# Performance work log

Hardware: AMD Instinct MI355X
Metric: run time of the kernel (lower is better)

The kernel has to match this reference:

```python
import jax, jax.numpy as jnp
import numpy as np

B, D, N = 4, 96, 512
ATTN = 256
OUT = 1


def setup_inputs() -> dict:
    key = jax.random.key(0)
    ks = jax.random.split(key, 4)
    x = jax.random.normal(ks[0], (B, D, N), dtype=jnp.float32)
    Wg1 = jax.random.normal(ks[1], (ATTN, D), dtype=jnp.float32) / np.sqrt(D)
    Wg2 = jax.random.normal(ks[2], (ATTN, D), dtype=jnp.float32) / np.sqrt(D)
    bg = jnp.zeros((ATTN,), dtype=jnp.float32)
    Wa_w = jax.random.normal(ks[3], (OUT, ATTN), dtype=jnp.float32) / np.sqrt(ATTN)
    Wa_b = jnp.zeros((OUT,), dtype=jnp.float32)
    ba = jnp.zeros((OUT,), dtype=jnp.float32)
    return {"x": x, "Wg1": Wg1, "Wg2": Wg2, "bg": bg, "Wa_w": Wa_w, "Wa_b": Wa_b, "ba": ba}


def reference(x, Wg1, Wg2, bg, Wa_w, Wa_b, ba):
    # x: (B, D, N) -> transpose to (B, N, D)
    xt = jnp.swapaxes(x, 1, 2)
    g1 = jnp.einsum("bnd,ad->bna", xt, Wg1)  # (B, N, ATTN)
    g2 = jnp.einsum("bnd,ad->bna", xt, Wg2)  # (B, N, ATTN)
    # pairwise additive scores: (B, N, N, ATTN)
    gnn = jnp.tanh(g1[:, :, None, :] + g2[:, None, :, :] + bg)
    # project to scalar per pair, add both biases (Wa bias and ba), sigmoid
    att = jax.nn.sigmoid(jnp.einsum("bnma,oa->bnmo", gnn, Wa_w) + Wa_b + ba)
    att = att.squeeze(-1)  # (B, N, N)
    return jnp.matmul(att, xt)  # (B, N, D)
```

## Files before the change

### kernel.cpp

```cpp
#include <hip/hip_runtime.h>
#include <math.h>

#define NB 4
#define ND 96
#define NN 512
#define NA 256

static constexpr float C_TANH = 2.8853900817779268f;
static constexpr float LOG2E  = 1.4426950408889634f;

__device__ __forceinline__ float fexp2(float x) {
#if __has_builtin(__builtin_amdgcn_exp2f)
  return __builtin_amdgcn_exp2f(x);
#else
  return exp2f(x);
#endif
}
__device__ __forceinline__ float frcp(float x) {
#if __has_builtin(__builtin_amdgcn_rcpf)
  return __builtin_amdgcn_rcpf(x);
#else
  return 1.0f / x;
#endif
}

__global__ __launch_bounds__(256) void k_prep(const float* __restrict__ Wg1,
                                              const float* __restrict__ Wg2,
                                              const float* __restrict__ Wa_w,
                                              const float* __restrict__ Wa_b,
                                              const float* __restrict__ ba,
                                              float* __restrict__ W1t,
                                              float* __restrict__ W2t,
                                              float* __restrict__ S0) {
  if (blockIdx.x == 192) {
    __shared__ float red[256];
    int t = threadIdx.x;
    red[t] = Wa_w[t];
    __syncthreads();
    for (int s = 128; s > 0; s >>= 1) {
      if (t < s) red[t] += red[t + s];
      __syncthreads();
    }
    if (t == 0) S0[0] = red[0] + Wa_b[0] + ba[0];
    return;
  }
  int idx = blockIdx.x * 256 + threadIdx.x;
  int mat = idx / (ND * NA);
  int rem = idx - mat * (ND * NA);
  int d = rem >> 8;
  int a = rem & 255;
  (mat ? W2t : W1t)[d * NA + a] = (mat ? Wg2 : Wg1)[a * ND + d];
}

__global__ __launch_bounds__(256, 2) void k_proj(const float* __restrict__ x,
                                                 const float* __restrict__ W1t,
                                                 const float* __restrict__ W2t,
                                                 const float* __restrict__ bg,
                                                 float* __restrict__ G1,
                                                 float* __restrict__ G2c,
                                                 float* __restrict__ xt) {
  __shared__ float4 xsh[ND];
  const int tid = threadIdx.x;
  const int b = blockIdx.x >> 7;
  const int n0 = (blockIdx.x & 127) * 4;

  for (int idx = tid; idx < ND * 4; idx += 256) {
    int d = idx >> 2, j = idx & 3;
    float v = x[(size_t)(b * ND + d) * NN + n0 + j];
    ((float*)&xsh[d])[j] = v;
    xt[(size_t)(b * NN + n0 + j) * ND + d] = v;
  }
  __syncthreads();

  const int a = tid;
  const float bgv = bg[a];
  float acc1[4], acc2[4];
#pragma unroll
  for (int j = 0; j < 4; ++j) { acc1[j] = bgv; acc2[j] = 0.f; }

  for (int d4 = 0; d4 < ND / 4; ++d4) {
    float w1[4], w2[4];
#pragma unroll
    for (int dd = 0; dd < 4; ++dd) {
      w1[dd] = W1t[(d4 * 4 + dd) * NA + a];
      w2[dd] = W2t[(d4 * 4 + dd) * NA + a];
    }
#pragma unroll
    for (int dd = 0; dd < 4; ++dd) {
      float4 xq = xsh[d4 * 4 + dd];
      float xv[4] = {xq.x, xq.y, xq.z, xq.w};
#pragma unroll
      for (int j = 0; j < 4; ++j) {
        acc1[j] = fmaf(w1[dd], xv[j], acc1[j]);
        acc2[j] = fmaf(w2[dd], xv[j], acc2[j]);
      }
    }
  }
  const int c = a >> 5, al = a & 31;
#pragma unroll
  for (int j = 0; j < 4; ++j) {
    G1[(size_t)(b * NN + n0 + j) * NA + a] = C_TANH * acc1[j];
    G2c[((size_t)(b * 8 + c) * NN + n0 + j) * 32 + al] = C_TANH * acc2[j];
  }
}

__global__ __launch_bounds__(256, 4) void k_main(const float* __restrict__ G1,
                                                 const float* __restrict__ G2c,
                                                 const float* __restrict__ xt,
                                                 const float* __restrict__ Wa_w,
                                                 const float* __restrict__ S0p,
                                                 float* __restrict__ out) {
  __shared__ float4 g2sh[256 * 8];
  __shared__ float attsh[4][NN];
  const int tid = threadIdx.x;
  const int b = blockIdx.x >> 7;
  const int n0 = (blockIdx.x & 127) << 2;
  const float S0 = S0p[0];
  const float4* __restrict__ W4 = (const float4*)Wa_w;
  const float* __restrict__ g1r0 = G1 + (size_t)(b * NN + n0) * NA;

  for (int p = 0; p < 2; ++p) {
    float acc[4] = {0.f, 0.f, 0.f, 0.f};
    for (int c = 0; c < 8; ++c) {
      const float4* __restrict__ src =
          (const float4*)(G2c + ((size_t)(b * 8 + c) * NN + p * 256) * 32);
      __syncthreads();
#pragma unroll
      for (int k = 0; k < 8; ++k) {
        int f = k * 256 + tid;
        int r = f >> 3, q = f & 7;
        g2sh[r * 8 + (q ^ (r & 7))] = src[f];
      }
      __syncthreads();
#pragma unroll
      for (int k4 = 0; k4 < 8; ++k4) {
        float4 v = g2sh[tid * 8 + (k4 ^ (tid & 7))];
        float g2v[4] = {v.x, v.y, v.z, v.w};
        float4 wq = W4[c * 8 + k4];
        float wv[4] = {wq.x, wq.y, wq.z, wq.w};
#pragma unroll
        for (int nl = 0; nl < 4; ++nl) {
          float4 g = *(const float4*)(g1r0 + nl * NA + c * 32 + k4 * 4);
          float g1v[4] = {g.x, g.y, g.z, g.w};
#pragma unroll
          for (int j = 0; j < 4; ++j) {
            float e = fexp2(g1v[j] + g2v[j]);
            acc[nl] = fmaf(wv[j], frcp(1.f + e), acc[nl]);
          }
        }
      }
    }
#pragma unroll
    for (int nl = 0; nl < 4; ++nl) {
      float z = S0 - 2.f * acc[nl];
      attsh[nl][p * 256 + tid] = frcp(1.f + fexp2(-LOG2E * z));
    }
  }
  __syncthreads();

  const int w = tid >> 6;
  const int l = tid & 63;
  const float* __restrict__ xb = xt + (size_t)b * NN * ND;
  const float* __restrict__ arow = attsh[w];
  float o0 = 0.f, o1 = 0.f;
  for (int m = 0; m < NN; ++m) {
    float av = arow[m];
    const float* xr = xb + m * ND;
    o0 = fmaf(av, xr[l], o0);
    o1 = fmaf(av, xr[64 + (l & 31)], o1);
  }
  float* orow = out + (size_t)(b * NN + n0 + w) * ND;
  orow[l] = o0;
  if (l < 32) orow[64 + l] = o1;
}

extern "C" void kernel_launch(void* const* d_in, const int* in_sizes, int n_in,
                              void* d_out, int out_size, void* d_ws, size_t ws_size,
                              hipStream_t stream) {
  const float* x    = (const float*)d_in[0];
  const float* Wg1  = (const float*)d_in[1];
  const float* Wg2  = (const float*)d_in[2];
  const float* bg   = (const float*)d_in[3];
  const float* Wa_w = (const float*)d_in[4];
  const float* Wa_b = (const float*)d_in[5];
  const float* ba   = (const float*)d_in[6];
  float* out = (float*)d_out;

  float* ws  = (float*)d_ws;
  float* G1  = ws;
  float* G2c = ws + 524288;
  float* xtw = ws + 1048576;
  float* W1t = ws + 1245184;
  float* W2t = ws + 1269760;
  float* S0  = ws + 1294336;

  hipLaunchKernelGGL(k_prep, dim3(193), dim3(256), 0, stream,
                     Wg1, Wg2, Wa_w, Wa_b, ba, W1t, W2t, S0);
  hipLaunchKernelGGL(k_proj, dim3(512), dim3(256), 0, stream,
                     x, W1t, W2t, bg, G1, G2c, xtw);
  hipLaunchKernelGGL(k_main, dim3(512), dim3(256), 0, stream,
                     G1, G2c, xtw, Wa_w, S0, out);
}
```

Measured before the change: 169.8 us.

## Split main kernel across m-quarters and attention halves with atomic output reduction

The weight-transpose prep kernel is removed. The projection kernel now reads Wg1/Wg2 rows directly as float4, and the Wa_w sum is computed inside the main kernel. The main kernel grid grows to four times as many blocks: each block handles a quarter of the m range, and its two thread halves each cover half of the attention dimension, reading G2 rows straight from global memory with no LDS staging. The two halves are combined through shared memory, and the partial att·x products are summed with atomicAdd into an output that is zeroed by a memset. This raises parallelism and occupancy, at the cost of extra atomics, a memset, and redundant per-thread weight sums.

```diff
diff --git a/kernel.cpp b/kernel.cpp
--- a/kernel.cpp
+++ b/kernel.cpp
@@ -24,40 +24,12 @@
 #endif
 }
 
-__global__ __launch_bounds__(256) void k_prep(const float* __restrict__ Wg1,
-                                              const float* __restrict__ Wg2,
-                                              const float* __restrict__ Wa_w,
-                                              const float* __restrict__ Wa_b,
-                                              const float* __restrict__ ba,
-                                              float* __restrict__ W1t,
-                                              float* __restrict__ W2t,
-                                              float* __restrict__ S0) {
-  if (blockIdx.x == 192) {
-    __shared__ float red[256];
-    int t = threadIdx.x;
-    red[t] = Wa_w[t];
-    __syncthreads();
-    for (int s = 128; s > 0; s >>= 1) {
-      if (t < s) red[t] += red[t + s];
-      __syncthreads();
-    }
-    if (t == 0) S0[0] = red[0] + Wa_b[0] + ba[0];
-    return;
-  }
-  int idx = blockIdx.x * 256 + threadIdx.x;
-  int mat = idx / (ND * NA);
-  int rem = idx - mat * (ND * NA);
-  int d = rem >> 8;
-  int a = rem & 255;
-  (mat ? W2t : W1t)[d * NA + a] = (mat ? Wg2 : Wg1)[a * ND + d];
-}
-
-__global__ __launch_bounds__(256, 2) void k_proj(const float* __restrict__ x,
-                                                 const float* __restrict__ W1t,
-                                                 const float* __restrict__ W2t,
+__global__ __launch_bounds__(256, 4) void k_proj(const float* __restrict__ x,
+                                                 const float* __restrict__ Wg1,
+                                                 const float* __restrict__ Wg2,
                                                  const float* __restrict__ bg,
                                                  float* __restrict__ G1,
-                                                 float* __restrict__ G2c,
+                                                 float* __restrict__ G2,
                                                  float* __restrict__ xt) {
   __shared__ float4 xsh[ND];
   const int tid = threadIdx.x;
@@ -66,81 +38,91 @@
 
   for (int idx = tid; idx < ND * 4; idx += 256) {
     int d = idx >> 2, j = idx & 3;
-    float v = x[(size_t)(b * ND + d) * NN + n0 + j];
-    ((float*)&xsh[d])[j] = v;
-    xt[(size_t)(b * NN + n0 + j) * ND + d] = v;
-  }
-  __syncthreads();
+    ((float*)&xsh[d])[j] = x[(size_t)(b * ND + d) * NN + n0 + j];
+  }
+  __syncthreads();
+  if (tid < ND) {
+    float4 v = xsh[tid];
+    xt[(size_t)(b * NN + n0 + 0) * ND + tid] = v.x;
+    xt[(size_t)(b * NN + n0 + 1) * ND + tid] = v.y;
+    xt[(size_t)(b * NN + n0 + 2) * ND + tid] = v.z;
+    xt[(size_t)(b * NN + n0 + 3) * ND + tid] = v.w;
+  }
 
   const int a = tid;
   const float bgv = bg[a];
-  float acc1[4], acc2[4];
-#pragma unroll
-  for (int j = 0; j < 4; ++j) { acc1[j] = bgv; acc2[j] = 0.f; }
-
+  float acc1[4] = {bgv, bgv, bgv, bgv};
+  float acc2[4] = {0.f, 0.f, 0.f, 0.f};
+  const float4* __restrict__ w1p = (const float4*)(Wg1 + (size_t)a * ND);
+  const float4* __restrict__ w2p = (const float4*)(Wg2 + (size_t)a * ND);
+
+#pragma unroll 4
   for (int d4 = 0; d4 < ND / 4; ++d4) {
-    float w1[4], w2[4];
-#pragma unroll
-    for (int dd = 0; dd < 4; ++dd) {
-      w1[dd] = W1t[(d4 * 4 + dd) * NA + a];
-      w2[dd] = W2t[(d4 * 4 + dd) * NA + a];
-    }
+    float4 w1 = w1p[d4], w2 = w2p[d4];
+    float w1c[4] = {w1.x, w1.y, w1.z, w1.w};
+    float w2c[4] = {w2.x, w2.y, w2.z, w2.w};
 #pragma unroll
     for (int dd = 0; dd < 4; ++dd) {
       float4 xq = xsh[d4 * 4 + dd];
       float xv[4] = {xq.x, xq.y, xq.z, xq.w};
 #pragma unroll
       for (int j = 0; j < 4; ++j) {
-        acc1[j] = fmaf(w1[dd], xv[j], acc1[j]);
-        acc2[j] = fmaf(w2[dd], xv[j], acc2[j]);
+        acc1[j] = fmaf(w1c[dd], xv[j], acc1[j]);
+        acc2[j] = fmaf(w2c[dd], xv[j], acc2[j]);
       }
     }
   }
-  const int c = a >> 5, al = a & 31;
 #pragma unroll
   for (int j = 0; j < 4; ++j) {
     G1[(size_t)(b * NN + n0 + j) * NA + a] = C_TANH * acc1[j];
-    G2c[((size_t)(b * 8 + c) * NN + n0 + j) * 32 + al] = C_TANH * acc2[j];
-  }
-}
-
-__global__ __launch_bounds__(256, 4) void k_main(const float* __restrict__ G1,
-                                                 const float* __restrict__ G2c,
+    G2[(size_t)(b * NN + n0 + j) * NA + a] = C_TANH * acc2[j];
+  }
+}
+
+__global__ __launch_bounds__(256, 8) void k_main(const float* __restrict__ G1,
+                                                 const float* __restrict__ G2,
                                                  const float* __restrict__ xt,
                                                  const float* __restrict__ Wa_w,
-                                                 const float* __restrict__ S0p,
+                                                 const float* __restrict__ Wa_b,
+                                                 const float* __restrict__ ba,
                                                  float* __restrict__ out) {
-  __shared__ float4 g2sh[256 * 8];
-  __shared__ float attsh[4][NN];
+  __shared__ float psum[2048];
+  __shared__ float attsh[512];
   const int tid = threadIdx.x;
-  const int b = blockIdx.x >> 7;
-  const int n0 = (blockIdx.x & 127) << 2;
-  const float S0 = S0p[0];
+  const int bid = blockIdx.x;
+  const int q  = bid & 3;
+  const int ng = (bid >> 2) & 127;
+  const int b  = bid >> 9;
+  const int n0 = ng * 4;
+  const int mloc = tid & 127;
+  const int ah = __builtin_amdgcn_readfirstlane(tid >> 7);
+  const int m = q * 128 + mloc;
+
   const float4* __restrict__ W4 = (const float4*)Wa_w;
   const float* __restrict__ g1r0 = G1 + (size_t)(b * NN + n0) * NA;
-
-  for (int p = 0; p < 2; ++p) {
-    float acc[4] = {0.f, 0.f, 0.f, 0.f};
-    for (int c = 0; c < 8; ++c) {
-      const float4* __restrict__ src =
-          (const float4*)(G2c + ((size_t)(b * 8 + c) * NN + p * 256) * 32);
-      __syncthreads();
-#pragma unroll
-      for (int k = 0; k < 8; ++k) {
-        int f = k * 256 + tid;
-        int r = f >> 3, q = f & 7;
-        g2sh[r * 8 + (q ^ (r & 7))] = src[f];
-      }
-      __syncthreads();
-#pragma unroll
-      for (int k4 = 0; k4 < 8; ++k4) {
-        float4 v = g2sh[tid * 8 + (k4 ^ (tid & 7))];
-        float g2v[4] = {v.x, v.y, v.z, v.w};
-        float4 wq = W4[c * 8 + k4];
+  const float* __restrict__ g2row = G2 + (size_t)(b * NN + m) * NA;
+
+  float acc[4] = {0.f, 0.f, 0.f, 0.f};
+  float sw = 0.f;
+
+#pragma unroll 1
+  for (int ci = 0; ci < 4; ++ci) {
+    const int c = ah * 4 + ci;
+    const float4* __restrict__ g2c4 = (const float4*)(g2row + c * 32);
+#pragma unroll
+    for (int h = 0; h < 2; ++h) {
+      float4 g2r[4];
+#pragma unroll
+      for (int i = 0; i < 4; ++i) g2r[i] = g2c4[h * 4 + i];
+#pragma unroll
+      for (int k4 = 0; k4 < 4; ++k4) {
+        float g2v[4] = {g2r[k4].x, g2r[k4].y, g2r[k4].z, g2r[k4].w};
+        float4 wq = W4[c * 8 + h * 4 + k4];
         float wv[4] = {wq.x, wq.y, wq.z, wq.w};
+        sw += (wv[0] + wv[1]) + (wv[2] + wv[3]);
 #pragma unroll
         for (int nl = 0; nl < 4; ++nl) {
-          float4 g = *(const float4*)(g1r0 + nl * NA + c * 32 + k4 * 4);
+          float4 g = *(const float4*)(g1r0 + nl * NA + c * 32 + (h * 4 + k4) * 4);
           float g1v[4] = {g.x, g.y, g.z, g.w};
 #pragma unroll
           for (int j = 0; j < 4; ++j) {
@@ -150,28 +132,61 @@
         }
       }
     }
+  }
+
+  float* accsh = psum;
+  float* swsh  = psum + 512;
+  if (ah == 1) {
+#pragma unroll
+    for (int nl = 0; nl < 4; ++nl) accsh[nl * 128 + mloc] = acc[nl];
+    swsh[mloc] = sw;
+  }
+  __syncthreads();
+  if (ah == 0) {
+    float bias = Wa_b[0] + ba[0];
+    float swt = sw + swsh[mloc] + bias;
 #pragma unroll
     for (int nl = 0; nl < 4; ++nl) {
-      float z = S0 - 2.f * acc[nl];
-      attsh[nl][p * 256 + tid] = frcp(1.f + fexp2(-LOG2E * z));
+      float z = swt - 2.f * (acc[nl] + accsh[nl * 128 + mloc]);
+      attsh[nl * 128 + mloc] = frcp(1.f + fexp2(-LOG2E * z));
     }
   }
   __syncthreads();
 
   const int w = tid >> 6;
   const int l = tid & 63;
-  const float* __restrict__ xb = xt + (size_t)b * NN * ND;
-  const float* __restrict__ arow = attsh[w];
-  float o0 = 0.f, o1 = 0.f;
-  for (int m = 0; m < NN; ++m) {
-    float av = arow[m];
-    const float* xr = xb + m * ND;
-    o0 = fmaf(av, xr[l], o0);
-    o1 = fmaf(av, xr[64 + (l & 31)], o1);
-  }
-  float* orow = out + (size_t)(b * NN + n0 + w) * ND;
-  orow[l] = o0;
-  if (l < 32) orow[64 + l] = o1;
+  float o0[4] = {0.f, 0.f, 0.f, 0.f};
+  float o1[4] = {0.f, 0.f, 0.f, 0.f};
+  const float* __restrict__ xb = xt + (size_t)(b * NN + q * 128 + w * 32) * ND;
+  for (int mi = 0; mi < 32; ++mi) {
+    const float* xr = xb + mi * ND;
+    float xv0 = xr[l];
+    float xv1 = xr[64 + (l & 31)];
+#pragma unroll
+    for (int nl = 0; nl < 4; ++nl) {
+      float av = attsh[nl * 128 + w * 32 + mi];
+      o0[nl] = fmaf(av, xv0, o0[nl]);
+      o1[nl] = fmaf(av, xv1, o1[nl]);
+    }
+  }
+  __syncthreads();
+#pragma unroll
+  for (int nl = 0; nl < 4; ++nl) {
+    psum[(w * 4 + nl) * 128 + l] = o0[nl];
+    if (l < 32) psum[(w * 4 + nl) * 128 + 64 + l] = o1[nl];
+  }
+  __syncthreads();
+#pragma unroll
+  for (int it = 0; it < 2; ++it) {
+    int idx = it * 256 + tid;
+    int nl = idx >> 7;
+    int d = idx & 127;
+    if (d < ND) {
+      float s = (psum[(0 + nl) * 128 + d] + psum[(4 + nl) * 128 + d]) +
+                (psum[(8 + nl) * 128 + d] + psum[(12 + nl) * 128 + d]);
+      atomicAdd(out + (size_t)(b * NN + n0 + nl) * ND + d, s);
+    }
+  }
 }
 
 extern "C" void kernel_launch(void* const* d_in, const int* in_sizes, int n_in,
@@ -188,16 +203,12 @@
 
   float* ws  = (float*)d_ws;
   float* G1  = ws;
-  float* G2c = ws + 524288;
+  float* G2  = ws + 524288;
   float* xtw = ws + 1048576;
-  float* W1t = ws + 1245184;
-  float* W2t = ws + 1269760;
-  float* S0  = ws + 1294336;
-
-  hipLaunchKernelGGL(k_prep, dim3(193), dim3(256), 0, stream,
-                     Wg1, Wg2, Wa_w, Wa_b, ba, W1t, W2t, S0);
+
+  hipMemsetAsync(out, 0, (size_t)out_size * sizeof(float), stream);
   hipLaunchKernelGGL(k_proj, dim3(512), dim3(256), 0, stream,
-                     x, W1t, W2t, bg, G1, G2c, xtw);
-  hipLaunchKernelGGL(k_main, dim3(512), dim3(256), 0, stream,
-                     G1, G2c, xtw, Wa_w, S0, out);
-}
+                     x, Wg1, Wg2, bg, G1, G2, xtw);
+  hipLaunchKernelGGL(k_main, dim3(2048), dim3(256), 0, stream,
+                     G1, G2, xtw, Wa_w, Wa_b, ba, out);
+}
```

New measurement: 227.6 us. +34.0%, slower.
